# Performance work log

Measured on AMD Instinct MI355X. Metric: run time of the kernel, lower is better.

## Reference

```python
import jax, jax.numpy as jnp
import numpy as np
from jax import lax

B, N = 2, 16384      # point clouds, points per cloud
S = 4096             # N * ratio (ratio = 0.25)
R = 0.1              # ball-query radius
K = 32               # max_num_neighbors
F_IN = 16            # input feature dim
NEG = jnp.float32(-1e30)


def fps_single(p):
    """Farthest point sampling on one cloud p:[N,3], deterministic start at 0 -> [S] int32 indices."""
    def step(carry, _):
        dmin, last = carry
        d = jnp.sum((p - p[last]) ** 2, axis=-1)
        dmin = jnp.minimum(dmin, d)
        nxt = jnp.argmax(dmin).astype(jnp.int32)
        return (dmin, nxt), nxt
    (_, _), rest = lax.scan(step, (jnp.full((N,), 1e10, jnp.float32), jnp.int32(0)), None, length=S - 1)
    return jnp.concatenate([jnp.zeros((1,), jnp.int32), rest])


def setup_inputs() -> dict:
    key = jax.random.key(0)
    ks = jax.random.split(key, 6)
    x = jax.random.normal(ks[0], (B * N, F_IN), jnp.float32)
    pos = jax.random.uniform(ks[1], (B * N, 3), jnp.float32)  # unit cube
    batch = (jnp.arange(B * N) // N).astype(jnp.int32)
    W1 = jax.random.normal(ks[2], (F_IN + 3, 64), jnp.float32) * float(1.0 / np.sqrt(F_IN + 3))
    b1 = jnp.zeros((64,), jnp.float32)
    W2 = jax.random.normal(ks[3], (64, 64), jnp.float32) * float(1.0 / np.sqrt(64))
    b2 = jnp.zeros((64,), jnp.float32)
    W3 = jax.random.normal(ks[4], (64, 128), jnp.float32) * float(1.0 / np.sqrt(64))
    b3 = jnp.zeros((128,), jnp.float32)
    return dict(x=x, pos=pos, batch=batch, W1=W1, b1=b1, W2=W2, b2=b2, W3=W3, b3=b3)


def reference(x, pos, batch, W1, b1, W2, b2, W3, b3):
    xb = x.reshape(B, N, F_IN)
    pb = pos.reshape(B, N, 3)
    idx = jax.vmap(fps_single)(pb)                                 # [B,S]
    centers = jnp.take_along_axis(pb, idx[..., None], axis=1)      # [B,S,3]
    # ball query: all points within R of each centroid, first K in index order
    d2 = jnp.sum((centers[:, :, None, :] - pb[:, None, :, :]) ** 2, axis=-1)  # [B,S,N]
    within = d2 <= R * R
    # PyG remove_self_loops on the bipartite edge_index (numeric global src == global dst)
    src_g = jnp.arange(B, dtype=jnp.int32)[:, None, None] * N + jnp.arange(N, dtype=jnp.int32)[None, None, :]
    dst_g = jnp.arange(B, dtype=jnp.int32)[:, None, None] * S + jnp.arange(S, dtype=jnp.int32)[None, :, None]
    within = within & (src_g != dst_g)
    cand = jnp.where(within, jnp.arange(N, dtype=jnp.int32)[None, None, :], N)
    nbr = jnp.sort(cand, axis=-1)[..., :K]                         # [B,S,K]
    valid = nbr < N
    nbr = jnp.minimum(nbr, N - 1)
    xj = jnp.take_along_axis(xb[:, None, :, :], nbr[..., None], axis=2)  # [B,S,K,F]
    pj = jnp.take_along_axis(pb[:, None, :, :], nbr[..., None], axis=2)  # [B,S,K,3]
    rel = pj - centers[:, :, None, :]
    # PyG add_self_loops: edge (d, d) for each global dst id d -> src is flat point index d
    dflat = jnp.arange(B, dtype=jnp.int32)[:, None] * S + jnp.arange(S, dtype=jnp.int32)[None, :]  # [B,S]
    feat_self = jnp.concatenate([x[dflat], pos[dflat] - centers], axis=-1)[:, :, None, :]  # [B,S,1,F+3]
    feats = jnp.concatenate([jnp.concatenate([xj, rel], axis=-1), feat_self], axis=2)      # [B,S,K+1,F+3]
    valid_all = jnp.concatenate([valid, jnp.ones((B, S, 1), bool)], axis=2)
    # PointNetConv local MLP (plain last layer) + max aggregation
    h = jax.nn.relu(feats @ W1 + b1)
    h = jax.nn.relu(h @ W2 + b2)
    h = h @ W3 + b3                                                # [B,S,K+1,128]
    h = jnp.where(valid_all[..., None], h, NEG)
    x_out = jnp.max(h, axis=2)                                     # [B,S,128]
    batch_out = (dflat // S).reshape(-1).astype(jnp.int32)
    return x_out.reshape(B * S, 128), centers.reshape(B * S, 3), batch_out
```

## Files before the change

### kernel.cpp

```cpp
#include <hip/hip_runtime.h>
#include <cstdint>
#include <cstddef>

#define BB 2
#define NN 16384
#define SS 4096
#define KK 32
#define FIN 16
#define R2C 0.01f
#define NCHUNK 256

typedef unsigned long long u64;

template <int CTRL>
__device__ __forceinline__ float fstep(float k) {
  const int n = __builtin_amdgcn_update_dpp(__float_as_int(k), __float_as_int(k),
                                            CTRL, 0xf, 0xf, false);
  return fmaxf(k, __int_as_float(n));
}
__device__ __forceinline__ float fchain(float k) {
  k = fstep<0x111>(k);
  k = fstep<0x112>(k);
  k = fstep<0x114>(k);
  k = fstep<0x118>(k);
  k = fstep<0x142>(k);
  k = fstep<0x143>(k);
  return k;
}
template <int CTRL>
__device__ __forceinline__ unsigned int ustep(unsigned int k) {
  const unsigned int n = (unsigned int)__builtin_amdgcn_update_dpp(
      (int)k, (int)k, CTRL, 0xf, 0xf, false);
  return k > n ? k : n;
}
__device__ __forceinline__ unsigned int uchain(unsigned int k) {
  k = ustep<0x111>(k);
  k = ustep<0x112>(k);
  k = ustep<0x114>(k);
  k = ustep<0x118>(k);
  k = ustep<0x142>(k);
  k = ustep<0x143>(k);
  return k;
}

template <int CTRL>
__device__ __forceinline__ double kstep64(double k) {
  const u64 kb = (u64)__double_as_longlong(k);
  const int lo = (int)(unsigned int)kb;
  const int hi = (int)(unsigned int)(kb >> 32);
  const int nlo = __builtin_amdgcn_update_dpp(lo, lo, CTRL, 0xf, 0xf, false);
  const int nhi = __builtin_amdgcn_update_dpp(hi, hi, CTRL, 0xf, 0xf, false);
  const double nk = __longlong_as_double(
      (long long)(((u64)(unsigned int)nhi << 32) | (unsigned int)nlo));
  return fmax(k, nk);
}
__device__ __forceinline__ double kchain64(double k) {
  k = kstep64<0x111>(k);
  k = kstep64<0x112>(k);
  k = kstep64<0x114>(k);
  k = kstep64<0x118>(k);
  k = kstep64<0x142>(k);
  k = kstep64<0x143>(k);
  return k;
}

__device__ __forceinline__ int part3(int x) {
  return (x & 1) | ((x & 2) << 2) | ((x & 4) << 4);
}

__global__ __launch_bounds__(512) void bin_kernel(const float* __restrict__ pos,
                                                  float4* __restrict__ cellpts,
                                                  float4* __restrict__ bboxLo,
                                                  float4* __restrict__ bboxHi) {
  const int b = blockIdx.x, t = threadIdx.x;
  const float* __restrict__ p = pos + (size_t)b * NN * 3;
  __shared__ int hist[512], sA[512], sB[512];
  hist[t] = 0;
  __syncthreads();
  int cidc[NN / 512];
#pragma unroll
  for (int m = 0; m < NN / 512; ++m) {
    const int i = m * 512 + t;
    const float x = p[i * 3 + 0], y = p[i * 3 + 1], z = p[i * 3 + 2];
    const int cx = min(7, (int)(x * 8.0f));
    const int cy = min(7, (int)(y * 8.0f));
    const int cz = min(7, (int)(z * 8.0f));
    const int cid = part3(cx) | (part3(cy) << 1) | (part3(cz) << 2);
    cidc[m] = cid;
    atomicAdd(&hist[cid], 1);
  }
  __syncthreads();
  sA[t] = hist[t];
  __syncthreads();
  int* src = sA;
  int* dst = sB;
  for (int off = 1; off < 512; off <<= 1) {
    int v = src[t];
    if (t >= off) v += src[t - off];
    dst[t] = v;
    __syncthreads();
    int* tmp = src; src = dst; dst = tmp;
  }
  const int excl = (t == 0) ? 0 : src[t - 1];
  __syncthreads();
  hist[t] = excl;
  __syncthreads();
#pragma unroll
  for (int m = 0; m < NN / 512; ++m) {
    const int i = m * 512 + t;
    const int slot = atomicAdd(&hist[cidc[m]], 1);
    cellpts[(size_t)b * NN + slot] =
        make_float4(p[i * 3 + 0], p[i * 3 + 1], p[i * 3 + 2], __int_as_float(i));
  }
  __threadfence_block();
  __syncthreads();
  if (t < NCHUNK) {
    float4 lo = make_float4(1e30f, 1e30f, 1e30f, 0.0f);
    float4 hi = make_float4(-1e30f, -1e30f, -1e30f, 0.0f);
    for (int k = 0; k < 64; ++k) {
      const float4 q = cellpts[(size_t)b * NN + t * 64 + k];
      lo.x = fminf(lo.x, q.x); lo.y = fminf(lo.y, q.y); lo.z = fminf(lo.z, q.z);
      hi.x = fmaxf(hi.x, q.x); hi.y = fmaxf(hi.y, q.y); hi.z = fmaxf(hi.z, q.z);
    }
    bboxLo[b * NCHUNK + t] = lo;
    bboxHi[b * NCHUNK + t] = hi;
  }
}

#define FPS_T 1024
#define FPS_NW 16

__global__ __launch_bounds__(FPS_T, 1) void fps_kernel(const float* __restrict__ pos,
                                                       const float4* __restrict__ cellpts,
                                                       const float4* __restrict__ bboxLo,
                                                       const float4* __restrict__ bboxHi,
                                                       int* __restrict__ idx_out) {
  const int b = blockIdx.x;
  const int t = threadIdx.x;
  const int wid = t >> 6;
  const int lane = t & 63;
  const float* __restrict__ p = pos + (size_t)b * NN * 3;
  const float4* __restrict__ cp = cellpts + (size_t)b * NN;

  __shared__ float sDmin[NN];
  __shared__ u64 sKey[2][NCHUNK];

  const int cown = ((lane & 15) << 4) | wid;
  const int slotOwn = (wid << 4) | (lane & 15);
  const float4 blo = bboxLo[b * NCHUNK + cown];
  const float4 bhi = bboxHi[b * NCHUNK + cown];

  float px[16], py[16], pz[16];
  unsigned int rp[16];
#pragma unroll
  for (int cc = 0; cc < 16; ++cc) {
    const int c = (cc << 4) | wid;
    const float4 q = cp[(size_t)((c << 6) + lane)];
    px[cc] = q.x; py[cc] = q.y; pz[cc] = q.z;
    const unsigned int pid = (unsigned int)__float_as_int(q.w);
    rp[cc] = ((16383u - pid) << 14) | ((unsigned int)c << 6) | (unsigned int)lane;
  }

  const u64 initKey = ((u64)(unsigned int)__float_as_int(1e30f) << 32);
  if (t < NCHUNK) sKey[0][t] = initKey;
  for (int s = t; s < NN; s += FPS_T) sDmin[s] = 1e10f;
  if (t == 0) idx_out[b * SS + 0] = 0;
  float lx = p[0], ly = p[1], lz = p[2];
  u64 kOwn = initKey;
  __syncthreads();

  int buf = 0;
  float* const sD0 = &sDmin[(wid << 6) + lane];

  for (int it = 1; it < SS; ++it) {
    const float mvOwn = __int_as_float((int)(unsigned int)(kOwn >> 32));
    const float ax = fmaxf(fmaxf(blo.x - lx, lx - bhi.x), 0.0f);
    const float ay = fmaxf(fmaxf(blo.y - ly, ly - bhi.y), 0.0f);
    const float az = fmaxf(fmaxf(blo.z - lz, lz - bhi.z), 0.0f);
    const float bl2 = ax * ax + ay * ay + az * az;
    const bool act = (lane < 16) && !(bl2 * 0.99999f > mvOwn);
    if ((lane < 16) && !act) sKey[buf ^ 1][slotOwn] = kOwn;
    const unsigned int mm = (unsigned int)__ballot(act);

#pragma unroll
    for (int cc = 0; cc < 16; ++cc) {
      if (mm & (1u << cc)) {
        const float od = sD0[cc * 1024];
        const float dx = px[cc] - lx, dy = py[cc] - ly, dz = pz[cc] - lz;
        const float d = __fadd_rn(__fadd_rn(__fmul_rn(dx, dx), __fmul_rn(dy, dy)),
                                  __fmul_rn(dz, dz));
        const float nd = fminf(od, d);
        sD0[cc * 1024] = nd;
        const float cm = fchain(nd);
        const float cm_s = __int_as_float(
            __builtin_amdgcn_readlane(__float_as_int(cm), 63));
        unsigned int tt = (nd == cm_s) ? rp[cc] : 0u;
        tt = uchain(tt);
        if (lane == 63) {
          const u64 key = ((u64)(unsigned int)__float_as_int(cm) << 32) | tt;
          sKey[buf ^ 1][(wid << 4) | cc] = key;
        }
      }
    }
    __syncthreads();
    buf ^= 1;

    kOwn = sKey[buf][slotOwn];
    double bk = 0.0;
#pragma unroll
    for (int g = 0; g < 4; ++g) {
      const double k = __longlong_as_double((long long)sKey[buf][g * 64 + lane]);
      bk = fmax(bk, k);
    }
    bk = kchain64(bk);
    const unsigned int lo63 = (unsigned int)__builtin_amdgcn_readlane(
        (int)(unsigned int)(u64)__double_as_longlong(bk), 63);
    const int fi = 16383 - (int)(lo63 >> 14);
    if (t == 0) idx_out[b * SS + it] = fi;
    lx = p[fi * 3 + 0];
    ly = p[fi * 3 + 1];
    lz = p[fi * 3 + 2];
  }
}

__global__ __launch_bounds__(256) void ballq_kernel(const float* __restrict__ pos,
                                                    const int* __restrict__ idx,
                                                    int* __restrict__ nbr,
                                                    int* __restrict__ cnt,
                                                    float* __restrict__ outC,
                                                    float* __restrict__ outB) {
  const int cs = blockIdx.x * 4 + (threadIdx.x >> 6);
  const int lane = threadIdx.x & 63;
  const int b = cs >> 12;
  const int s = cs & (SS - 1);
  const float* __restrict__ p = pos + (size_t)b * NN * 3;
  const int ci = idx[cs];
  const float cx = p[ci * 3 + 0], cy = p[ci * 3 + 1], cz = p[ci * 3 + 2];
  const int excl = (b == 0) ? s : -1;
  int count = 0;
  for (int tile = 0; tile < NN / 64; ++tile) {
    const int i = tile * 64 + lane;
    const float dx = cx - p[i * 3 + 0];
    const float dy = cy - p[i * 3 + 1];
    const float dz = cz - p[i * 3 + 2];
    const float d2 = __fadd_rn(__fadd_rn(__fmul_rn(dx, dx), __fmul_rn(dy, dy)), __fmul_rn(dz, dz));
    const bool in = (d2 <= R2C) && (i != excl);
    const unsigned long long m = __ballot(in);
    if (in) {
      const int rank = count + (int)__popcll(m & ((1ull << lane) - 1ull));
      if (rank < KK) nbr[cs * KK + rank] = i;
    }
    count += (int)__popcll(m);
    if (count >= KK) break;
  }
  if (lane == 0) {
    cnt[cs] = count < KK ? count : KK;
    outC[cs * 3 + 0] = cx;
    outC[cs * 3 + 1] = cy;
    outC[cs * 3 + 2] = cz;
    outB[cs] = (float)b;
  }
}

#define EE 33
__global__ __launch_bounds__(128) void mlp_kernel(const float* __restrict__ x,
                                                  const float* __restrict__ pos,
                                                  const int* __restrict__ nbr,
                                                  const int* __restrict__ cnt,
                                                  const float* __restrict__ W1,
                                                  const float* __restrict__ b1,
                                                  const float* __restrict__ W2,
                                                  const float* __restrict__ b2,
                                                  const float* __restrict__ W3,
                                                  const float* __restrict__ b3,
                                                  const float* __restrict__ outC,
                                                  float* __restrict__ outX) {
  __shared__ float sF[EE][20];
  __shared__ float sH1[EE][64];
  __shared__ float sH2[EE][64];
  __shared__ int sValid[EE];

  const int cs = blockIdx.x;
  const int tid = threadIdx.x;
  const int b = cs >> 12;
  const int c = tid & 63;
  const int half = tid >> 6;

  float w1c[19], w2c[64], w3c[64];
#pragma unroll
  for (int k = 0; k < 19; ++k) w1c[k] = W1[k * 64 + c];
#pragma unroll
  for (int k = 0; k < 64; ++k) w2c[k] = W2[k * 64 + c];
#pragma unroll
  for (int k = 0; k < 64; ++k) w3c[k] = W3[k * 128 + tid];
  const float b1c = b1[c], b2c = b2[c], b3c = b3[tid];

  if (tid < EE) {
    const float ccx = outC[cs * 3 + 0], ccy = outC[cs * 3 + 1], ccz = outC[cs * 3 + 2];
    int row;
    bool valid;
    if (tid < KK) {
      const int cn = cnt[cs];
      valid = tid < cn;
      const int j = valid ? nbr[cs * KK + tid] : 0;
      row = b * NN + j;
    } else {
      valid = true;
      row = cs;
    }
    for (int f = 0; f < FIN; ++f) sF[tid][f] = x[(size_t)row * FIN + f];
    sF[tid][16] = pos[(size_t)row * 3 + 0] - ccx;
    sF[tid][17] = pos[(size_t)row * 3 + 1] - ccy;
    sF[tid][18] = pos[(size_t)row * 3 + 2] - ccz;
    sValid[tid] = valid ? 1 : 0;
  }
  __syncthreads();
  for (int e = half; e < EE; e += 2) {
    float acc = b1c;
#pragma unroll
    for (int k = 0; k < 19; ++k) acc += sF[e][k] * w1c[k];
    sH1[e][c] = fmaxf(acc, 0.0f);
  }
  __syncthreads();
  for (int e = half; e < EE; e += 2) {
    float acc = b2c;
#pragma unroll
    for (int k = 0; k < 64; ++k) acc += sH1[e][k] * w2c[k];
    sH2[e][c] = fmaxf(acc, 0.0f);
  }
  __syncthreads();
  float mx = -1e30f;
  for (int e = 0; e < EE; ++e) {
    if (sValid[e]) {
      float acc = b3c;
#pragma unroll
      for (int k = 0; k < 64; ++k) acc += sH2[e][k] * w3c[k];
      mx = fmaxf(mx, acc);
    }
  }
  outX[(size_t)cs * 128 + tid] = mx;
}

extern "C" void kernel_launch(void* const* d_in, const int* in_sizes, int n_in,
                              void* d_out, int out_size, void* d_ws, size_t ws_size,
                              hipStream_t stream) {
  const float* x = (const float*)d_in[0];
  const float* pos = (const float*)d_in[1];
  const float* W1 = (const float*)d_in[3];
  const float* b1 = (const float*)d_in[4];
  const float* W2 = (const float*)d_in[5];
  const float* b2 = (const float*)d_in[6];
  const float* W3 = (const float*)d_in[7];
  const float* b3 = (const float*)d_in[8];

  float* out = (float*)d_out;
  float* outX = out;
  float* outC = out + (size_t)BB * SS * 128;
  float* outB = outC + (size_t)BB * SS * 3;

  float4* cellpts = (float4*)d_ws;
  float4* bboxLo = cellpts + (size_t)BB * NN;
  float4* bboxHi = bboxLo + BB * NCHUNK;
  int* idx = (int*)(bboxHi + BB * NCHUNK);
  int* nbr = idx + BB * SS;
  int* cnt = nbr + (size_t)BB * SS * KK;

  hipLaunchKernelGGL(bin_kernel, dim3(BB), dim3(512), 0, stream, pos, cellpts, bboxLo, bboxHi);
  hipLaunchKernelGGL(fps_kernel, dim3(BB), dim3(FPS_T), 0, stream, pos, cellpts, bboxLo, bboxHi, idx);
  hipLaunchKernelGGL(ballq_kernel, dim3(BB * SS / 4), dim3(256), 0, stream,
                     pos, idx, nbr, cnt, outC, outB);
  hipLaunchKernelGGL(mlp_kernel, dim3(BB * SS), dim3(128), 0, stream,
                     x, pos, nbr, cnt, W1, b1, W2, b2, W3, b3, outC, outX);
}
```

Baseline: 4.765 ms.

## Keep FPS min-distances in registers and batch chunk keys via writelane

```diff
diff --git a/kernel.cpp b/kernel.cpp
--- a/kernel.cpp
+++ b/kernel.cpp
@@ -142,15 +142,14 @@
   const float* __restrict__ p = pos + (size_t)b * NN * 3;
   const float4* __restrict__ cp = cellpts + (size_t)b * NN;
 
-  __shared__ float sDmin[NN];
-  __shared__ u64 sKey[2][NCHUNK];
+  __shared__ __align__(16) u64 sKey[2][NCHUNK];
 
   const int cown = ((lane & 15) << 4) | wid;
   const int slotOwn = (wid << 4) | (lane & 15);
   const float4 blo = bboxLo[b * NCHUNK + cown];
   const float4 bhi = bboxHi[b * NCHUNK + cown];
 
-  float px[16], py[16], pz[16];
+  float px[16], py[16], pz[16], dmn[16];
   unsigned int rp[16];
 #pragma unroll
   for (int cc = 0; cc < 16; ++cc) {
@@ -159,18 +158,17 @@
     px[cc] = q.x; py[cc] = q.y; pz[cc] = q.z;
     const unsigned int pid = (unsigned int)__float_as_int(q.w);
     rp[cc] = ((16383u - pid) << 14) | ((unsigned int)c << 6) | (unsigned int)lane;
+    dmn[cc] = 1e10f;
   }
 
   const u64 initKey = ((u64)(unsigned int)__float_as_int(1e30f) << 32);
   if (t < NCHUNK) sKey[0][t] = initKey;
-  for (int s = t; s < NN; s += FPS_T) sDmin[s] = 1e10f;
   if (t == 0) idx_out[b * SS + 0] = 0;
   float lx = p[0], ly = p[1], lz = p[2];
   u64 kOwn = initKey;
   __syncthreads();
 
   int buf = 0;
-  float* const sD0 = &sDmin[(wid << 6) + lane];
 
   for (int it = 1; it < SS; ++it) {
     const float mvOwn = __int_as_float((int)(unsigned int)(kOwn >> 32));
@@ -179,47 +177,52 @@
     const float az = fmaxf(fmaxf(blo.z - lz, lz - bhi.z), 0.0f);
     const float bl2 = ax * ax + ay * ay + az * az;
     const bool act = (lane < 16) && !(bl2 * 0.99999f > mvOwn);
-    if ((lane < 16) && !act) sKey[buf ^ 1][slotOwn] = kOwn;
     const unsigned int mm = (unsigned int)__ballot(act);
 
-#pragma unroll
-    for (int cc = 0; cc < 16; ++cc) {
-      if (mm & (1u << cc)) {
-        const float od = sD0[cc * 1024];
-        const float dx = px[cc] - lx, dy = py[cc] - ly, dz = pz[cc] - lz;
-        const float d = __fadd_rn(__fadd_rn(__fmul_rn(dx, dx), __fmul_rn(dy, dy)),
-                                  __fmul_rn(dz, dz));
-        const float nd = fminf(od, d);
-        sD0[cc * 1024] = nd;
-        const float cm = fchain(nd);
-        const float cm_s = __int_as_float(
-            __builtin_amdgcn_readlane(__float_as_int(cm), 63));
-        unsigned int tt = (nd == cm_s) ? rp[cc] : 0u;
-        tt = uchain(tt);
-        if (lane == 63) {
-          const u64 key = ((u64)(unsigned int)__float_as_int(cm) << 32) | tt;
-          sKey[buf ^ 1][(wid << 4) | cc] = key;
-        }
-      }
-    }
+    int vhi = (int)(unsigned int)(kOwn >> 32);
+    int vlo = (int)(unsigned int)kOwn;
+
+#define BODY(cc)                                                                 \
+    if (mm & (1u << cc)) {                                                       \
+      const float dx = px[cc] - lx, dy = py[cc] - ly, dz = pz[cc] - lz;          \
+      const float d = __fadd_rn(__fadd_rn(__fmul_rn(dx, dx), __fmul_rn(dy, dy)), \
+                                __fmul_rn(dz, dz));                              \
+      const float nd = fminf(dmn[cc], d);                                        \
+      dmn[cc] = nd;                                                              \
+      const float cm = fchain(nd);                       \
+      const int cmb = __builtin_amdgcn_readlane(__float_as_int(cm), 63);         \
+      unsigned int tt = (nd == __int_as_float(cmb)) ? rp[cc] : 0u;               \
+      tt = uchain(tt);           \
+      const int tts = __builtin_amdgcn_readlane((int)tt, 63);                    \
+      asm("v_writelane_b32 %0, %1, " #cc : "+v"(vhi) : "s"(cmb));                \
+      asm("v_writelane_b32 %0, %1, " #cc : "+v"(vlo) : "s"(tts));                \
+    }
+    BODY(0) BODY(1) BODY(2) BODY(3) BODY(4) BODY(5) BODY(6) BODY(7)
+    BODY(8) BODY(9) BODY(10) BODY(11) BODY(12) BODY(13) BODY(14) BODY(15)
+#undef BODY
+
+    if (lane < 16)
+      sKey[buf ^ 1][slotOwn] = ((u64)(unsigned int)vhi << 32) | (unsigned int)vlo;
     __syncthreads();
     buf ^= 1;
 
     kOwn = sKey[buf][slotOwn];
-    double bk = 0.0;
-#pragma unroll
-    for (int g = 0; g < 4; ++g) {
-      const double k = __longlong_as_double((long long)sKey[buf][g * 64 + lane]);
-      bk = fmax(bk, k);
-    }
+    const ulonglong2 ka = *(const ulonglong2*)&sKey[buf][2 * lane];
+    const ulonglong2 kb = *(const ulonglong2*)&sKey[buf][128 + 2 * lane];
+    double bk = fmax(fmax(__longlong_as_double((long long)ka.x),
+                          __longlong_as_double((long long)ka.y)),
+                     fmax(__longlong_as_double((long long)kb.x),
+                          __longlong_as_double((long long)kb.y)));
     bk = kchain64(bk);
     const unsigned int lo63 = (unsigned int)__builtin_amdgcn_readlane(
         (int)(unsigned int)(u64)__double_as_longlong(bk), 63);
     const int fi = 16383 - (int)(lo63 >> 14);
     if (t == 0) idx_out[b * SS + it] = fi;
-    lx = p[fi * 3 + 0];
-    ly = p[fi * 3 + 1];
-    lz = p[fi * 3 + 2];
+    const int slot = (int)(lo63 & 0x3FFFu);
+    const float4 wq = cp[(size_t)slot];
+    lx = wq.x;
+    ly = wq.y;
+    lz = wq.z;
   }
 }
 
```

Measured after the change: 4.614 ms. -3.2%, faster.
